# Optimization experiments

Measured on AMD Instinct MI355X. Metric: run time of the kernel, lower is better.

Reference implementation:

```python
import jax, jax.numpy as jnp
import numpy as np

NQ = 4096
N0, N1 = 32768, 8192
N = N0 + N1
F = 128          # emb_dim (32x0e+32x1e)
H = 4            # num_heads
HD = F // H
NB = 64          # fc_neurons[0] radial basis size
DEG = 32
CUTOFFS = jnp.array([2.0, 4.0], dtype=jnp.float32)
OFFSETS = jnp.array([0.1, 0.2], dtype=jnp.float32)


def _sph_harm(u):
    # component-normalized real spherical harmonics l=0,1,2 of unit vectors u [E,3]
    x, y, z = u[:, 0], u[:, 1], u[:, 2]
    s3, s15, s5 = 3.0 ** 0.5, 15.0 ** 0.5, 5.0 ** 0.5
    return jnp.stack([
        jnp.ones_like(x),
        s3 * x, s3 * y, s3 * z,
        s15 * x * y, s15 * y * z, 0.5 * s5 * (3.0 * z * z - 1.0),
        s15 * x * z, 0.5 * s15 * (x * x - y * y),
    ], axis=-1)  # [E,9]


def setup_inputs() -> dict:
    key = jax.random.key(0)
    ks = jax.random.split(key, 20)
    E0 = NQ * DEG
    E1 = NQ * DEG
    edge_src = jnp.concatenate([
        jax.random.randint(ks[0], (E0,), 0, N0),
        jax.random.randint(ks[1], (E1,), N0, N),
    ])
    edge_dst = jnp.concatenate([
        jax.random.randint(ks[2], (E0,), 0, NQ),
        jax.random.randint(ks[3], (E1,), 0, NQ),
    ])
    scale_id = jnp.concatenate([jnp.zeros((E0,), jnp.int32), jnp.ones((E1,), jnp.int32)])
    r = lambda k, sh, s=1.0: jax.random.normal(k, sh, jnp.float32) * s
    return {
        'query_coord': r(ks[4], (NQ, 3)),
        'node_feature': r(ks[5], (N, F)),
        'node_coord': r(ks[6], (N, 3)),
        'edge_src': edge_src, 'edge_dst': edge_dst, 'scale_id': scale_id,
        'b_dst': r(ks[7], (F,)),
        'Wq': r(ks[8], (F, F), F ** -0.5),
        'Wk': r(ks[9], (F, F), F ** -0.5),
        'Wv': r(ks[10], (F, F), F ** -0.5),
        'Wo': r(ks[11], (F, F), F ** -0.5),
        'bo': r(ks[12], (F,)),
        'W_rad0': r(ks[13], (NB, NB), NB ** -0.5), 'b_rad0': r(ks[14], (NB,)),
        'W_rad1': r(ks[15], (NB, NB), NB ** -0.5), 'b_rad1': r(ks[16], (NB,)),
        'W_msg': r(ks[17], (NB, F), NB ** -0.5),
        'W_sh': r(ks[18], (9, F), 9 ** -0.5),
        'W_alpha': r(ks[19], (NB, H), NB ** -0.5),
    }


def _forward(query_coord, node_feature, node_coord, b_dst, Wq, Wk, Wv, Wo, bo,
             W_rad0, b_rad0, W_rad1, b_rad1, W_msg, W_sh, W_alpha,
             edge_src, edge_dst, scale_id):
    Nq = query_coord.shape[0]
    vec = node_coord[edge_src] - query_coord[edge_dst]            # [E,3]
    rlen = jnp.sqrt(jnp.sum(vec * vec, -1) + 1e-12)               # [E]
    off = OFFSETS[scale_id]
    cut = CUTOFFS[scale_id]
    xn = (rlen - off) / (cut - off)                               # normalized radius per scale
    centers = jnp.linspace(0.0, 1.0, NB)
    std = 1.0 / NB
    g = jnp.exp(-0.5 * ((xn[:, None] - centers) / std) ** 2)      # [E,NB] gaussian RBF
    soft = 0.5 * (1.0 + jnp.cos(jnp.pi * jnp.clip((xn - 0.8) / 0.2, 0.0, 1.0)))
    g = g * soft[:, None]                                         # soft finite cutoff
    # per-scale Linear after radial basis (2 scales, masked select)
    edge_scalar = jnp.where((scale_id == 0)[:, None], g @ W_rad0 + b_rad0, g @ W_rad1 + b_rad1)
    sh = _sph_harm(vec / rlen[:, None])                           # [E,9]
    # attention GNN (equiformer-style): dst features start as zeros + learned bias
    q = (b_dst @ Wq).reshape(H, HD)
    k = (node_feature @ Wk)[edge_src].reshape(-1, H, HD)
    logits = jnp.einsum('hd,ehd->eh', q, k) / (HD ** 0.5) + edge_scalar @ W_alpha  # [E,H]
    m = jax.ops.segment_max(logits, edge_dst, num_segments=Nq)
    p = jnp.exp(logits - m[edge_dst])
    denom = jax.ops.segment_sum(p, edge_dst, num_segments=Nq)
    alpha = p / (denom[edge_dst] + 1e-9)                          # segment softmax [E,H]
    v_e = (node_feature @ Wv)[edge_src] * (edge_scalar @ W_msg) + sh @ W_sh  # [E,F]
    msg = (alpha[:, :, None] * v_e.reshape(-1, H, HD)).reshape(-1, F)
    out = jax.ops.segment_sum(msg, edge_dst, num_segments=Nq)     # [Nq,F]
    return out @ Wo + bo


def reference(query_coord, node_feature, node_coord, edge_src, edge_dst, scale_id,
              b_dst, Wq, Wk, Wv, Wo, bo, W_rad0, b_rad0, W_rad1, b_rad1,
              W_msg, W_sh, W_alpha):
    return _forward(query_coord, node_feature, node_coord, b_dst, Wq, Wk, Wv, Wo, bo,
                    W_rad0, b_rad0, W_rad1, b_rad1, W_msg, W_sh, W_alpha,
                    edge_src, edge_dst, scale_id)
```

## Files before the change

### kernel.cpp

```cpp
#include <hip/hip_runtime.h>
#include <hip/hip_bf16.h>
#include <math.h>

#define PI_F 3.14159265358979323846f

typedef __attribute__((ext_vector_type(8))) short short8v;
typedef __attribute__((ext_vector_type(4))) float f32x4;

__device__ __forceinline__ short f2bf(float x) {
    return __builtin_bit_cast(short, __float2bfloat16(x));
}
__device__ __forceinline__ float bf2f(unsigned short u) {
    return __uint_as_float(((unsigned)u) << 16);
}
__device__ __forceinline__ int pack_bf2(float a, float b) {
    return (int)(unsigned short)f2bf(a) | ((int)(unsigned short)f2bf(b) << 16);
}

static const size_t WS_WA     = 0;
static const size_t WS_BA     = 512;
static const size_t WS_BM     = 520;
static const size_t WS_WMF    = 776;
static const size_t WS_WSHF   = 8968;
static const size_t WS_QKF    = 11016;
static const size_t WS_WVF    = 12040;
static const size_t WS_WOF    = 20232;
static const size_t WS_COUNTS = 28424;
static const size_t WS_OFFS   = 36624;
static const size_t WS_CURSOR = 44824;
static const size_t WS_PACKED = 53016;
static const size_t WS_LK     = 315160;
static const size_t WS_EDP    = 479000;
static const size_t WS_EDG    = 1527576;
static const size_t WS_VB     = 2576152;
static const size_t WS_OUTPRE = 5197592;

__global__ __launch_bounds__(256) void k_prepfmt(
    const float* b_dst, const float* Wq, const float* Wk,
    const float* W_rad0, const float* b_rad0,
    const float* W_rad1, const float* b_rad1,
    const float* W_msg, const float* W_alpha, const float* Wv,
    const float* Wo, const float* W_sh,
    const int* edge_dst, const int* scale_id,
    float* Wa, float* ba, float* bm,
    short* WmF, short* WshF, short* QKF, short* WVF, short* WOF,
    int* counts, int E, int NQr) {
    __shared__ float qs_s[128];
    __shared__ float qk_s[512];
    int t = threadIdx.x;
    int b = blockIdx.x;
    if (b == 0) {
        if (t < 128) {
            float acc = 0.f;
            for (int c = 0; c < 128; ++c) acc += b_dst[c] * Wq[c * 128 + t];
            qs_s[t] = acc;
        }
        __syncthreads();
        if (t < 128) {
            const float invs = 0.17677669529663687f;
            for (int h = 0; h < 4; ++h) {
                float acc = 0.f;
                for (int d = 0; d < 32; ++d)
                    acc += Wk[t * 128 + h * 32 + d] * qs_s[h * 32 + d];
                qk_s[t * 4 + h] = acc * invs;
            }
        }
        for (int idx = t; idx < 512; idx += 256) {
            int s = idx >> 8, i = (idx >> 2) & 63, h = idx & 3;
            const float* Wr = s ? W_rad1 : W_rad0;
            float acc = 0.f;
            for (int u = 0; u < 64; ++u) acc += Wr[i * 64 + u] * W_alpha[u * 4 + h];
            Wa[idx] = acc;
        }
        if (t < 8) {
            int s = t >> 2, h = t & 3;
            const float* br = s ? b_rad1 : b_rad0;
            float acc = 0.f;
            for (int u = 0; u < 64; ++u) acc += br[u] * W_alpha[u * 4 + h];
            ba[t] = acc;
        }
        {
            int s = t >> 7, c = t & 127;
            const float* br = s ? b_rad1 : b_rad0;
            float acc = 0.f;
            for (int u = 0; u < 64; ++u) acc += br[u] * W_msg[u * 128 + c];
            bm[t] = acc;
        }
        __syncthreads();
        for (int idx = t; idx < 2048; idx += 256) {
            int j = idx & 7, lane = (idx >> 3) & 63, kh = idx >> 9;
            int k = kh * 32 + ((lane >> 4) << 3) + j;
            int col = lane & 15;
            QKF[idx] = f2bf(col < 4 ? qk_s[k * 4 + col] : 0.f);
        }
    } else if (b <= 208) {
        int item = (b - 1) * 256 + t;
        if (item < 16384) {
            int j = item & 7, lane = (item >> 3) & 63, kh = (item >> 9) & 1;
            int ct = (item >> 10) & 7, sid = item >> 13;
            int k = kh * 32 + ((lane >> 4) << 3) + j;
            int c = (lane & 15) * 8 + ct;
            const float* Wr = sid ? W_rad1 : W_rad0;
            float acc = 0.f;
            for (int u = 0; u < 64; ++u) acc += Wr[k * 64 + u] * W_msg[u * 128 + c];
            WmF[item] = f2bf(acc);
        } else if (item < 20480) {
            int i2 = item - 16384;
            int j = i2 & 7, lane = (i2 >> 3) & 63, ct = (i2 >> 9) & 7;
            int k = ((lane >> 4) << 3) + j;
            int c = (lane & 15) * 8 + ct;
            WshF[i2] = f2bf(k < 9 ? W_sh[k * 128 + c] : 0.f);
        } else if (item < 36864) {
            int i2 = item - 20480;
            int j = i2 & 7, lane = (i2 >> 3) & 63, ct = (i2 >> 9) & 7, kh = (i2 >> 12) & 3;
            int k = kh * 32 + ((lane >> 4) << 3) + j;
            int c = (lane & 15) * 8 + ct;
            WVF[i2] = f2bf(Wv[k * 128 + c]);
        } else {
            int i2 = item - 36864;
            int j = i2 & 7, lane = (i2 >> 3) & 63, ct = (i2 >> 9) & 7, kh = (i2 >> 12) & 3;
            int k = kh * 32 + ((lane >> 4) << 3) + j;
            int c = (lane & 15) * 8 + ct;
            WOF[i2] = f2bf(Wo[k * 128 + c]);
        }
    } else {
        int e = (b - 209) * 256 + t;
        if (e < E) atomicAdd(&counts[scale_id[e] * NQr + edge_dst[e]], 1);
    }
}

template <typename OUT, bool LK>
__global__ __launch_bounds__(256) void k_mgemm(
    const float* A, const short* WF, const float* bias, OUT* out,
    float* lk, const short* QKF, int M) {
    int t = threadIdx.x;
    int w = t >> 6, lane = t & 63;
    int m = lane & 15, grp = lane >> 4;
    int row0 = (blockIdx.x * 4 + w) * 16;
    if (row0 >= M) return;

    short8v a[4];
#pragma unroll
    for (int kh = 0; kh < 4; ++kh) {
        const float* ap = &A[(size_t)(row0 + m) * 128 + kh * 32 + grp * 8];
        float4 f0 = *(const float4*)ap;
        float4 f1 = *(const float4*)(ap + 4);
        a[kh][0] = f2bf(f0.x); a[kh][1] = f2bf(f0.y);
        a[kh][2] = f2bf(f0.z); a[kh][3] = f2bf(f0.w);
        a[kh][4] = f2bf(f1.x); a[kh][5] = f2bf(f1.y);
        a[kh][6] = f2bf(f1.z); a[kh][7] = f2bf(f1.w);
    }
    if constexpr (LK) {
        f32x4 cl = {0.f, 0.f, 0.f, 0.f};
#pragma unroll
        for (int kh = 0; kh < 4; ++kh) {
            short8v qb = *(const short8v*)&QKF[(kh * 64 + lane) * 8];
            cl = __builtin_amdgcn_mfma_f32_16x16x32_bf16(a[kh], qb, cl, 0, 0, 0);
        }
        if (m < 4) {
#pragma unroll
            for (int r = 0; r < 4; ++r)
                lk[(size_t)(row0 + grp * 4 + r) * 4 + m] = cl[r];
        }
    }
    f32x4 c8[8];
#pragma unroll
    for (int ct = 0; ct < 8; ++ct) {
        f32x4 c = {0.f, 0.f, 0.f, 0.f};
#pragma unroll
        for (int kh = 0; kh < 4; ++kh) {
            short8v bf = *(const short8v*)&WF[((kh * 8 + ct) * 64 + lane) * 8];
            c = __builtin_amdgcn_mfma_f32_16x16x32_bf16(a[kh], bf, c, 0, 0, 0);
        }
        c8[ct] = c;
    }
    if constexpr (sizeof(OUT) == 2) {
#pragma unroll
        for (int r = 0; r < 4; ++r) {
            int row = row0 + grp * 4 + r;
            int4 sv;
            sv.x = pack_bf2(c8[0][r], c8[1][r]);
            sv.y = pack_bf2(c8[2][r], c8[3][r]);
            sv.z = pack_bf2(c8[4][r], c8[5][r]);
            sv.w = pack_bf2(c8[6][r], c8[7][r]);
            *(int4*)&out[(size_t)row * 128 + m * 8] = sv;
        }
    } else {
        float4 b0 = make_float4(0.f, 0.f, 0.f, 0.f), b1 = b0;
        if (bias) {
            b0 = *(const float4*)&bias[m * 8];
            b1 = *(const float4*)&bias[m * 8 + 4];
        }
#pragma unroll
        for (int r = 0; r < 4; ++r) {
            int row = row0 + grp * 4 + r;
            float4 o0 = make_float4(c8[0][r] + b0.x, c8[1][r] + b0.y,
                                    c8[2][r] + b0.z, c8[3][r] + b0.w);
            float4 o1 = make_float4(c8[4][r] + b1.x, c8[5][r] + b1.y,
                                    c8[6][r] + b1.z, c8[7][r] + b1.w);
            *(float4*)&out[(size_t)row * 128 + m * 8] = o0;
            *(float4*)&out[(size_t)row * 128 + m * 8 + 4] = o1;
        }
    }
}

__global__ void k_scan(const int* counts, int* offsets, int* cursor, int nkey) {
    __shared__ int sdata[256];
    int t = threadIdx.x;
    int chunk = (nkey + 255) / 256;
    int sum = 0;
    for (int i = 0; i < chunk; ++i) {
        int idx = t * chunk + i;
        sum += (idx < nkey) ? counts[idx] : 0;
    }
    sdata[t] = sum;
    __syncthreads();
    for (int off = 1; off < 256; off <<= 1) {
        int v = (t >= off) ? sdata[t - off] : 0;
        __syncthreads();
        sdata[t] += v;
        __syncthreads();
    }
    int run = sdata[t] - sum;
    for (int i = 0; i < chunk; ++i) {
        int idx = t * chunk + i;
        if (idx < nkey) {
            offsets[idx] = run;
            cursor[idx] = run;
            run += counts[idx];
        }
    }
    if (t == 255) offsets[nkey] = sdata[255];
}

__global__ __launch_bounds__(256) void k_scatter_edge(
    const int* edge_src, const int* edge_dst, const int* scale_id,
    const float* qc, const float* nc, const float* lk,
    const float* WaB, const float* baB, int* cursor,
    int* packed, float* edP, float* edG, int E, int NQr) {
    __shared__ float WaS[512];
    __shared__ float baS[8];
    int t = threadIdx.x;
    for (int i = t; i < 512; i += 256) WaS[i] = WaB[i];
    if (t < 8) baS[t] = baB[t];
    __syncthreads();
    int e = blockIdx.x * 256 + t;
    if (e >= E) return;
    int src = edge_src[e], dst = edge_dst[e], sid = scale_id[e];
    int pos = atomicAdd(&cursor[sid * NQr + dst], 1);

    float qx = qc[dst * 3 + 0], qy = qc[dst * 3 + 1], qz = qc[dst * 3 + 2];
    float vx = nc[src * 3 + 0] - qx;
    float vy = nc[src * 3 + 1] - qy;
    float vz = nc[src * 3 + 2] - qz;
    float r = sqrtf(vx * vx + vy * vy + vz * vz + 1e-12f);
    float rinv = 1.0f / r;
    float ux = vx * rinv, uy = vy * rinv, uz = vz * rinv;

    float roff = sid ? 0.2f : 0.1f;
    float rdiv = sid ? (1.0f / 3.8f) : (1.0f / 1.9f);
    float xn = (r - roff) * rdiv;
    float su = fminf(fmaxf((xn - 0.8f) * 5.0f, 0.0f), 1.0f);
    float soft = 0.5f * (1.0f + __cosf(PI_F * su));

    float4 lkv = *(const float4*)&lk[(size_t)src * 4];

    const float qs = 64.f / 63.f;
    const float Qc = __expf(-qs * qs);
    const float* Wrow = WaS + sid * 256;
    float a0 = 0.f, a1 = 0.f, a2 = 0.f, a3 = 0.f;
#pragma unroll
    for (int ch = 0; ch < 8; ++ch) {
        float d = (xn - (float)(ch * 8) * (1.0f / 63.0f)) * 64.0f;
        float g = __expf(-0.5f * d * d);
        float tt = __expf(fminf(qs * d - 0.5f * qs * qs, 60.f));
#pragma unroll
        for (int j = 0; j < 8; ++j) {
            float4 wa = *(const float4*)&Wrow[(ch * 8 + j) * 4];
            a0 = fmaf(g, wa.x, a0);
            a1 = fmaf(g, wa.y, a1);
            a2 = fmaf(g, wa.z, a2);
            a3 = fmaf(g, wa.w, a3);
            g *= tt; tt *= Qc;
        }
    }
    float p0 = __expf(lkv.x + soft * a0 + baS[sid * 4 + 0]);
    float p1 = __expf(lkv.y + soft * a1 + baS[sid * 4 + 1]);
    float p2 = __expf(lkv.z + soft * a2 + baS[sid * 4 + 2]);
    float p3 = __expf(lkv.w + soft * a3 + baS[sid * 4 + 3]);
    packed[pos] = src | (dst << 16);
    *(float4*)&edP[(size_t)pos * 4] = make_float4(p0, p1, p2, p3);
    *(float4*)&edG[(size_t)pos * 4] = make_float4(ux, uy, uz, xn);
}

__device__ __forceinline__ short8v gchain(float xn, int k0, float soft, float Qc) {
    const float qs = 64.f / 63.f;
    float d = (xn - (float)k0 * (1.0f / 63.0f)) * 64.0f;
    float g = __expf(-0.5f * d * d);
    float tt = __expf(fminf(qs * d - 0.5f * qs * qs, 60.f));
    short8v rr;
#pragma unroll
    for (int j = 0; j < 8; ++j) {
        rr[j] = f2bf(g * soft);
        g *= tt; tt *= Qc;
    }
    return rr;
}

__global__ __launch_bounds__(256) void k_main7(
    const int* offsets, const int* packed, const float* edP, const float* edG,
    const unsigned short* Vu, const float* bm, const short* WmF, const short* WshF,
    float* out_pre, int NQr) {
    int t = threadIdx.x;
    int w = t >> 6, lane = t & 63;
    int dst = blockIdx.x * 4 + w;
    if (dst >= NQr) return;
    int m = lane & 15, grp = lane >> 4;
    int h = m >> 2;

    int s0a = offsets[dst],       s1a = offsets[dst + 1];
    int s0b = offsets[NQr + dst], s1b = offsets[NQr + dst + 1];
    int nt0 = (s1a - s0a + 15) >> 4;
    int nt1 = (s1b - s0b + 15) >> 4;
    int ntot = nt0 + nt1;

    float acc[8];
#pragma unroll
    for (int i = 0; i < 8; ++i) acc[i] = 0.f;
    float den = 0.f;

    float4 bmA0 = *(const float4*)&bm[m * 8];
    float4 bmA1 = *(const float4*)&bm[m * 8 + 4];
    float4 bmB0 = *(const float4*)&bm[128 + m * 8];
    float4 bmB1 = *(const float4*)&bm[128 + m * 8 + 4];

    const float qs = 64.f / 63.f;
    const float Qc = __expf(-qs * qs);
    const float s3 = 1.7320508075688772f, s15 = 3.872983346207417f, s5 = 2.23606797749979f;

    if (ntot > 0) {
        auto load_tile = [&](int tl, int& sid_o, float4& G4o, float (&pho)[4], int4 (&vvo)[4]) {
            int sid = (tl >= nt0) ? 1 : 0;
            int q0  = sid ? (s0b + (tl - nt0) * 16) : (s0a + tl * 16);
            int lim = sid ? s1b : s1a;
            int posA = q0 + m; if (posA >= lim) posA = lim - 1;
            G4o = *(const float4*)&edG[(size_t)posA * 4];
            int srcs[4];
#pragma unroll
            for (int r = 0; r < 4; ++r) {
                int pos = q0 + grp * 4 + r;
                bool valid = pos < lim;
                if (!valid) pos = lim - 1;
                srcs[r] = packed[pos] & 0xFFFF;
                float p = edP[(size_t)pos * 4 + h];
                pho[r] = valid ? p : 0.f;
            }
#pragma unroll
            for (int r = 0; r < 4; ++r)
                vvo[r] = *(const int4*)&Vu[(size_t)srcs[r] * 128 + m * 8];
            sid_o = sid;
        };

        int sidc; float4 G4c; float phc[4]; int4 vvc[4];
        load_tile(0, sidc, G4c, phc, vvc);

        for (int tl = 0; tl < ntot; ++tl) {
            bool hasNext = (tl + 1) < ntot;
            int sidn; float4 G4n; float phn[4]; int4 vvn[4];
            if (hasNext) load_tile(tl + 1, sidn, G4n, phn, vvn);

            int wds[4][4] = {{vvc[0].x, vvc[0].y, vvc[0].z, vvc[0].w},
                             {vvc[1].x, vvc[1].y, vvc[1].z, vvc[1].w},
                             {vvc[2].x, vvc[2].y, vvc[2].z, vvc[2].w},
                             {vvc[3].x, vvc[3].y, vvc[3].z, vvc[3].w}};
            den += phc[0] + phc[1] + phc[2] + phc[3];

            float bmv[8];
            {
                float4 b0 = sidc ? bmB0 : bmA0;
                float4 b1 = sidc ? bmB1 : bmA1;
                bmv[0] = b0.x; bmv[1] = b0.y; bmv[2] = b0.z; bmv[3] = b0.w;
                bmv[4] = b1.x; bmv[5] = b1.y; bmv[6] = b1.z; bmv[7] = b1.w;
            }
            const short* wmp = WmF + sidc * 8192;

            float xn = G4c.w;
            float su = fminf(fmaxf((xn - 0.8f) * 5.0f, 0.0f), 1.0f);
            float soft = 0.5f * (1.0f + __cosf(PI_F * su));
            short8v aG0 = gchain(xn, grp * 8, soft, Qc);
            short8v aG1 = gchain(xn, 32 + grp * 8, soft, Qc);

            float ux = G4c.x, uy = G4c.y, uz = G4c.z;
            float sh[9];
            sh[0] = 1.f; sh[1] = s3 * ux; sh[2] = s3 * uy; sh[3] = s3 * uz;
            sh[4] = s15 * ux * uy; sh[5] = s15 * uy * uz;
            sh[6] = 0.5f * s5 * (3.f * uz * uz - 1.f);
            sh[7] = s15 * ux * uz; sh[8] = 0.5f * s15 * (ux * ux - uy * uy);
            short8v aS;
#pragma unroll
            for (int j = 0; j < 8; ++j) {
                float v = (grp == 0) ? sh[j] : ((grp == 1 && j == 0) ? sh[8] : 0.f);
                aS[j] = f2bf(v);
            }

#pragma unroll
            for (int ct = 0; ct < 8; ++ct) {
                short8v b0 = *(const short8v*)&wmp[((ct * 2 + 0) * 64 + lane) * 8];
                short8v b1 = *(const short8v*)&wmp[((ct * 2 + 1) * 64 + lane) * 8];
                short8v bS = *(const short8v*)&WshF[(ct * 64 + lane) * 8];
                f32x4 cms = {0.f, 0.f, 0.f, 0.f};
                cms = __builtin_amdgcn_mfma_f32_16x16x32_bf16(aG0, b0, cms, 0, 0, 0);
                cms = __builtin_amdgcn_mfma_f32_16x16x32_bf16(aG1, b1, cms, 0, 0, 0);
                f32x4 csh = {0.f, 0.f, 0.f, 0.f};
                csh = __builtin_amdgcn_mfma_f32_16x16x32_bf16(aS, bS, csh, 0, 0, 0);
#pragma unroll
                for (int r = 0; r < 4; ++r) {
                    int word = wds[r][ct >> 1];
                    unsigned short vu = (ct & 1) ? (unsigned short)(word >> 16)
                                                 : (unsigned short)(word & 0xFFFF);
                    float vf = bf2f(vu);
                    float ve = fmaf(vf, cms[r] + bmv[ct], csh[r]);
                    acc[ct] = fmaf(phc[r], ve, acc[ct]);
                }
            }

            if (hasNext) {
                sidc = sidn; G4c = G4n;
#pragma unroll
                for (int r = 0; r < 4; ++r) { phc[r] = phn[r]; vvc[r] = vvn[r]; }
            }
        }
    }

#pragma unroll
    for (int i = 0; i < 8; ++i) {
        acc[i] += __shfl_xor(acc[i], 16);
        acc[i] += __shfl_xor(acc[i], 32);
    }
    den += __shfl_xor(den, 16);
    den += __shfl_xor(den, 32);
    if (lane < 16) {
        float dinv = 1.0f / (den + 1e-9f);
        float4 o0 = make_float4(acc[0] * dinv, acc[1] * dinv, acc[2] * dinv, acc[3] * dinv);
        float4 o1 = make_float4(acc[4] * dinv, acc[5] * dinv, acc[6] * dinv, acc[7] * dinv);
        *(float4*)&out_pre[(size_t)dst * 128 + m * 8] = o0;
        *(float4*)&out_pre[(size_t)dst * 128 + m * 8 + 4] = o1;
    }
}

extern "C" void kernel_launch(void* const* d_in, const int* in_sizes, int n_in,
                              void* d_out, int out_size, void* d_ws, size_t ws_size,
                              hipStream_t stream) {
    const float* query_coord = (const float*)d_in[0];
    const float* node_feature = (const float*)d_in[1];
    const float* node_coord = (const float*)d_in[2];
    const int* edge_src = (const int*)d_in[3];
    const int* edge_dst = (const int*)d_in[4];
    const int* scale_id = (const int*)d_in[5];
    const float* b_dst = (const float*)d_in[6];
    const float* Wq = (const float*)d_in[7];
    const float* Wk = (const float*)d_in[8];
    const float* Wv = (const float*)d_in[9];
    const float* Wo = (const float*)d_in[10];
    const float* bo = (const float*)d_in[11];
    const float* W_rad0 = (const float*)d_in[12];
    const float* b_rad0 = (const float*)d_in[13];
    const float* W_rad1 = (const float*)d_in[14];
    const float* b_rad1 = (const float*)d_in[15];
    const float* W_msg = (const float*)d_in[16];
    const float* W_sh = (const float*)d_in[17];
    const float* W_alpha = (const float*)d_in[18];
    (void)n_in; (void)ws_size; (void)out_size;

    int NQr = in_sizes[0] / 3;
    int Nn = in_sizes[1] / 128;
    int E = in_sizes[3];
    int nkey = NQr * 2;

    float* ws = (float*)d_ws;
    float* Wa = ws + WS_WA;
    float* ba = ws + WS_BA;
    float* bm = ws + WS_BM;
    short* WmF = (short*)(ws + WS_WMF);
    short* WshF = (short*)(ws + WS_WSHF);
    short* QKF = (short*)(ws + WS_QKF);
    short* WVF = (short*)(ws + WS_WVF);
    short* WOF = (short*)(ws + WS_WOF);
    int* counts = (int*)(ws + WS_COUNTS);
    int* offsets = (int*)(ws + WS_OFFS);
    int* cursor = (int*)(ws + WS_CURSOR);
    int* packed = (int*)(ws + WS_PACKED);
    float* lk = ws + WS_LK;
    float* edP = ws + WS_EDP;
    float* edG = ws + WS_EDG;
    unsigned short* Vb = (unsigned short*)(ws + WS_VB);
    float* out_pre = ws + WS_OUTPRE;
    float* out = (float*)d_out;

    hipMemsetAsync(counts, 0, nkey * sizeof(int), stream);
    int histBlocks = (E + 255) / 256;
    hipLaunchKernelGGL(k_prepfmt, dim3(209 + histBlocks), dim3(256), 0, stream,
                       b_dst, Wq, Wk, W_rad0, b_rad0, W_rad1, b_rad1, W_msg, W_alpha,
                       Wv, Wo, W_sh, edge_dst, scale_id,
                       Wa, ba, bm, WmF, WshF, QKF, WVF, WOF, counts, E, NQr);
    hipLaunchKernelGGL((k_mgemm<unsigned short, true>), dim3((Nn + 63) / 64), dim3(256), 0,
                       stream, node_feature, WVF, (const float*)nullptr, Vb, lk, QKF, Nn);
    hipLaunchKernelGGL(k_scan, dim3(1), dim3(256), 0, stream, counts, offsets, cursor, nkey);
    hipLaunchKernelGGL(k_scatter_edge, dim3((E + 255) / 256), dim3(256), 0, stream,
                       edge_src, edge_dst, scale_id, query_coord, node_coord, lk,
                       Wa, ba, cursor, packed, edP, edG, E, NQr);
    hipLaunchKernelGGL(k_main7, dim3((NQr + 3) / 4), dim3(256), 0, stream,
                       offsets, packed, edP, edG, Vb, bm, WmF, WshF, out_pre, NQr);
    hipLaunchKernelGGL((k_mgemm<float, false>), dim3((NQr + 63) / 64), dim3(256), 0, stream,
                       out_pre, WOF, bo, out, (float*)nullptr, (const short*)nullptr, NQr);
}
```

Before: 147.0 us.

## Split per-destination edge loop into independent 16-edge tiles with atomic accumulation

```diff
diff --git a/kernel.cpp b/kernel.cpp
--- a/kernel.cpp
+++ b/kernel.cpp
@@ -28,12 +28,15 @@
 static const size_t WS_COUNTS = 28424;
 static const size_t WS_OFFS   = 36624;
 static const size_t WS_CURSOR = 44824;
-static const size_t WS_PACKED = 53016;
-static const size_t WS_LK     = 315160;
-static const size_t WS_EDP    = 479000;
-static const size_t WS_EDG    = 1527576;
-static const size_t WS_VB     = 2576152;
-static const size_t WS_OUTPRE = 5197592;
+static const size_t WS_TCNT   = 53016;
+static const size_t WS_TMAP   = 53024;
+static const size_t WS_PACKED = 77608;
+static const size_t WS_LK     = 339752;
+static const size_t WS_EDP    = 503592;
+static const size_t WS_EDG    = 1552168;
+static const size_t WS_VB     = 2600744;
+static const size_t WS_OACC   = 5222184;
+static const size_t WS_DACC   = 5746472;
 
 __global__ __launch_bounds__(256) void k_prepfmt(
     const float* b_dst, const float* Wq, const float* Wk,
@@ -129,26 +132,36 @@
     }
 }
 
-template <typename OUT, bool LK>
+template <typename OUT, bool LK, bool DIV>
 __global__ __launch_bounds__(256) void k_mgemm(
     const float* A, const short* WF, const float* bias, OUT* out,
-    float* lk, const short* QKF, int M) {
+    float* lk, const short* QKF, const float* den, int M) {
     int t = threadIdx.x;
     int w = t >> 6, lane = t & 63;
     int m = lane & 15, grp = lane >> 4;
     int row0 = (blockIdx.x * 4 + w) * 16;
     if (row0 >= M) return;
 
+    float dinv[4] = {1.f, 1.f, 1.f, 1.f};
+    if constexpr (DIV) {
+        float4 dv = *(const float4*)&den[(size_t)(row0 + m) * 4];
+        dinv[0] = 1.f / (dv.x + 1e-9f);
+        dinv[1] = 1.f / (dv.y + 1e-9f);
+        dinv[2] = 1.f / (dv.z + 1e-9f);
+        dinv[3] = 1.f / (dv.w + 1e-9f);
+    }
+
     short8v a[4];
 #pragma unroll
     for (int kh = 0; kh < 4; ++kh) {
         const float* ap = &A[(size_t)(row0 + m) * 128 + kh * 32 + grp * 8];
         float4 f0 = *(const float4*)ap;
         float4 f1 = *(const float4*)(ap + 4);
-        a[kh][0] = f2bf(f0.x); a[kh][1] = f2bf(f0.y);
-        a[kh][2] = f2bf(f0.z); a[kh][3] = f2bf(f0.w);
-        a[kh][4] = f2bf(f1.x); a[kh][5] = f2bf(f1.y);
-        a[kh][6] = f2bf(f1.z); a[kh][7] = f2bf(f1.w);
+        float s = dinv[kh];
+        a[kh][0] = f2bf(f0.x * s); a[kh][1] = f2bf(f0.y * s);
+        a[kh][2] = f2bf(f0.z * s); a[kh][3] = f2bf(f0.w * s);
+        a[kh][4] = f2bf(f1.x * s); a[kh][5] = f2bf(f1.y * s);
+        a[kh][6] = f2bf(f1.z * s); a[kh][7] = f2bf(f1.w * s);
     }
     if constexpr (LK) {
         f32x4 cl = {0.f, 0.f, 0.f, 0.f};
@@ -204,16 +217,19 @@
     }
 }
 
-__global__ void k_scan(const int* counts, int* offsets, int* cursor, int nkey) {
+__global__ void k_scan(const int* counts, int* offsets, int* cursor,
+                       int* tcnt, int* tileMap, int nkey) {
     __shared__ int sdata[256];
     int t = threadIdx.x;
     int chunk = (nkey + 255) / 256;
-    int sum = 0;
+    int se = 0, st = 0;
     for (int i = 0; i < chunk; ++i) {
         int idx = t * chunk + i;
-        sum += (idx < nkey) ? counts[idx] : 0;
-    }
-    sdata[t] = sum;
+        int c = (idx < nkey) ? counts[idx] : 0;
+        se += c;
+        st += (c + 15) >> 4;
+    }
+    sdata[t] = se;
     __syncthreads();
     for (int off = 1; off < 256; off <<= 1) {
         int v = (t >= off) ? sdata[t - off] : 0;
@@ -221,16 +237,32 @@
         sdata[t] += v;
         __syncthreads();
     }
-    int run = sdata[t] - sum;
+    int run_e = sdata[t] - se;
+    int tot_e = sdata[255];
+    __syncthreads();
+    sdata[t] = st;
+    __syncthreads();
+    for (int off = 1; off < 256; off <<= 1) {
+        int v = (t >= off) ? sdata[t - off] : 0;
+        __syncthreads();
+        sdata[t] += v;
+        __syncthreads();
+    }
+    int run_t = sdata[t] - st;
+    int tot_t = sdata[255];
     for (int i = 0; i < chunk; ++i) {
         int idx = t * chunk + i;
         if (idx < nkey) {
-            offsets[idx] = run;
-            cursor[idx] = run;
-            run += counts[idx];
-        }
-    }
-    if (t == 255) offsets[nkey] = sdata[255];
+            int c = counts[idx];
+            offsets[idx] = run_e;
+            cursor[idx] = run_e;
+            int nt = (c + 15) >> 4;
+            for (int j = 0; j < nt; ++j) tileMap[run_t + j] = idx | (j << 16);
+            run_e += c;
+            run_t += nt;
+        }
+    }
+    if (t == 0) { offsets[nkey] = tot_e; tcnt[0] = tot_t; }
 }
 
 __global__ __launch_bounds__(256) void k_scatter_edge(
@@ -307,128 +339,93 @@
     return rr;
 }
 
-__global__ __launch_bounds__(256) void k_main7(
+__global__ __launch_bounds__(256) void k_main8(
     const int* offsets, const int* packed, const float* edP, const float* edG,
     const unsigned short* Vu, const float* bm, const short* WmF, const short* WshF,
-    float* out_pre, int NQr) {
+    const int* tcnt, const int* tileMap,
+    float* out_acc, float* den_acc, int NQr) {
     int t = threadIdx.x;
     int w = t >> 6, lane = t & 63;
-    int dst = blockIdx.x * 4 + w;
-    if (dst >= NQr) return;
+    int T = blockIdx.x * 4 + w;
+    if (T >= tcnt[0]) return;
+    int mt = tileMap[T];
+    int key = mt & 0xFFFF, ti = mt >> 16;
+    int sid = (key >= NQr) ? 1 : 0;
+    int dst = key - (sid ? NQr : 0);
+    int q0 = offsets[key] + ti * 16;
+    int lim = offsets[key + 1];
     int m = lane & 15, grp = lane >> 4;
     int h = m >> 2;
 
-    int s0a = offsets[dst],       s1a = offsets[dst + 1];
-    int s0b = offsets[NQr + dst], s1b = offsets[NQr + dst + 1];
-    int nt0 = (s1a - s0a + 15) >> 4;
-    int nt1 = (s1b - s0b + 15) >> 4;
-    int ntot = nt0 + nt1;
-
-    float acc[8];
-#pragma unroll
-    for (int i = 0; i < 8; ++i) acc[i] = 0.f;
-    float den = 0.f;
-
-    float4 bmA0 = *(const float4*)&bm[m * 8];
-    float4 bmA1 = *(const float4*)&bm[m * 8 + 4];
-    float4 bmB0 = *(const float4*)&bm[128 + m * 8];
-    float4 bmB1 = *(const float4*)&bm[128 + m * 8 + 4];
+    int posA = q0 + m; if (posA >= lim) posA = lim - 1;
+    float4 G4 = *(const float4*)&edG[(size_t)posA * 4];
+    int srcs[4]; float ph[4];
+#pragma unroll
+    for (int r = 0; r < 4; ++r) {
+        int pos = q0 + grp * 4 + r;
+        bool valid = pos < lim;
+        if (!valid) pos = lim - 1;
+        srcs[r] = packed[pos] & 0xFFFF;
+        float p = edP[(size_t)pos * 4 + h];
+        ph[r] = valid ? p : 0.f;
+    }
+    int wds[4][4];
+#pragma unroll
+    for (int r = 0; r < 4; ++r) {
+        int4 vv = *(const int4*)&Vu[(size_t)srcs[r] * 128 + m * 8];
+        wds[r][0] = vv.x; wds[r][1] = vv.y; wds[r][2] = vv.z; wds[r][3] = vv.w;
+    }
+
+    float4 bm0 = *(const float4*)&bm[sid * 128 + m * 8];
+    float4 bm1 = *(const float4*)&bm[sid * 128 + m * 8 + 4];
+    float bmv[8] = {bm0.x, bm0.y, bm0.z, bm0.w, bm1.x, bm1.y, bm1.z, bm1.w};
+    const short* wmp = WmF + sid * 8192;
 
     const float qs = 64.f / 63.f;
     const float Qc = __expf(-qs * qs);
+    float xn = G4.w;
+    float su = fminf(fmaxf((xn - 0.8f) * 5.0f, 0.0f), 1.0f);
+    float soft = 0.5f * (1.0f + __cosf(PI_F * su));
+    short8v aG0 = gchain(xn, grp * 8, soft, Qc);
+    short8v aG1 = gchain(xn, 32 + grp * 8, soft, Qc);
+
     const float s3 = 1.7320508075688772f, s15 = 3.872983346207417f, s5 = 2.23606797749979f;
-
-    if (ntot > 0) {
-        auto load_tile = [&](int tl, int& sid_o, float4& G4o, float (&pho)[4], int4 (&vvo)[4]) {
-            int sid = (tl >= nt0) ? 1 : 0;
-            int q0  = sid ? (s0b + (tl - nt0) * 16) : (s0a + tl * 16);
-            int lim = sid ? s1b : s1a;
-            int posA = q0 + m; if (posA >= lim) posA = lim - 1;
-            G4o = *(const float4*)&edG[(size_t)posA * 4];
-            int srcs[4];
-#pragma unroll
-            for (int r = 0; r < 4; ++r) {
-                int pos = q0 + grp * 4 + r;
-                bool valid = pos < lim;
-                if (!valid) pos = lim - 1;
-                srcs[r] = packed[pos] & 0xFFFF;
-                float p = edP[(size_t)pos * 4 + h];
-                pho[r] = valid ? p : 0.f;
-            }
-#pragma unroll
-            for (int r = 0; r < 4; ++r)
-                vvo[r] = *(const int4*)&Vu[(size_t)srcs[r] * 128 + m * 8];
-            sid_o = sid;
-        };
-
-        int sidc; float4 G4c; float phc[4]; int4 vvc[4];
-        load_tile(0, sidc, G4c, phc, vvc);
-
-        for (int tl = 0; tl < ntot; ++tl) {
-            bool hasNext = (tl + 1) < ntot;
-            int sidn; float4 G4n; float phn[4]; int4 vvn[4];
-            if (hasNext) load_tile(tl + 1, sidn, G4n, phn, vvn);
-
-            int wds[4][4] = {{vvc[0].x, vvc[0].y, vvc[0].z, vvc[0].w},
-                             {vvc[1].x, vvc[1].y, vvc[1].z, vvc[1].w},
-                             {vvc[2].x, vvc[2].y, vvc[2].z, vvc[2].w},
-                             {vvc[3].x, vvc[3].y, vvc[3].z, vvc[3].w}};
-            den += phc[0] + phc[1] + phc[2] + phc[3];
-
-            float bmv[8];
-            {
-                float4 b0 = sidc ? bmB0 : bmA0;
-                float4 b1 = sidc ? bmB1 : bmA1;
-                bmv[0] = b0.x; bmv[1] = b0.y; bmv[2] = b0.z; bmv[3] = b0.w;
-                bmv[4] = b1.x; bmv[5] = b1.y; bmv[6] = b1.z; bmv[7] = b1.w;
-            }
-            const short* wmp = WmF + sidc * 8192;
-
-            float xn = G4c.w;
-            float su = fminf(fmaxf((xn - 0.8f) * 5.0f, 0.0f), 1.0f);
-            float soft = 0.5f * (1.0f + __cosf(PI_F * su));
-            short8v aG0 = gchain(xn, grp * 8, soft, Qc);
-            short8v aG1 = gchain(xn, 32 + grp * 8, soft, Qc);
-
-            float ux = G4c.x, uy = G4c.y, uz = G4c.z;
-            float sh[9];
-            sh[0] = 1.f; sh[1] = s3 * ux; sh[2] = s3 * uy; sh[3] = s3 * uz;
-            sh[4] = s15 * ux * uy; sh[5] = s15 * uy * uz;
-            sh[6] = 0.5f * s5 * (3.f * uz * uz - 1.f);
-            sh[7] = s15 * ux * uz; sh[8] = 0.5f * s15 * (ux * ux - uy * uy);
-            short8v aS;
-#pragma unroll
-            for (int j = 0; j < 8; ++j) {
-                float v = (grp == 0) ? sh[j] : ((grp == 1 && j == 0) ? sh[8] : 0.f);
-                aS[j] = f2bf(v);
-            }
-
-#pragma unroll
-            for (int ct = 0; ct < 8; ++ct) {
-                short8v b0 = *(const short8v*)&wmp[((ct * 2 + 0) * 64 + lane) * 8];
-                short8v b1 = *(const short8v*)&wmp[((ct * 2 + 1) * 64 + lane) * 8];
-                short8v bS = *(const short8v*)&WshF[(ct * 64 + lane) * 8];
-                f32x4 cms = {0.f, 0.f, 0.f, 0.f};
-                cms = __builtin_amdgcn_mfma_f32_16x16x32_bf16(aG0, b0, cms, 0, 0, 0);
-                cms = __builtin_amdgcn_mfma_f32_16x16x32_bf16(aG1, b1, cms, 0, 0, 0);
-                f32x4 csh = {0.f, 0.f, 0.f, 0.f};
-                csh = __builtin_amdgcn_mfma_f32_16x16x32_bf16(aS, bS, csh, 0, 0, 0);
-#pragma unroll
-                for (int r = 0; r < 4; ++r) {
-                    int word = wds[r][ct >> 1];
-                    unsigned short vu = (ct & 1) ? (unsigned short)(word >> 16)
-                                                 : (unsigned short)(word & 0xFFFF);
-                    float vf = bf2f(vu);
-                    float ve = fmaf(vf, cms[r] + bmv[ct], csh[r]);
-                    acc[ct] = fmaf(phc[r], ve, acc[ct]);
-                }
-            }
-
-            if (hasNext) {
-                sidc = sidn; G4c = G4n;
-#pragma unroll
-                for (int r = 0; r < 4; ++r) { phc[r] = phn[r]; vvc[r] = vvn[r]; }
-            }
+    float ux = G4.x, uy = G4.y, uz = G4.z;
+    float sh[9];
+    sh[0] = 1.f; sh[1] = s3 * ux; sh[2] = s3 * uy; sh[3] = s3 * uz;
+    sh[4] = s15 * ux * uy; sh[5] = s15 * uy * uz;
+    sh[6] = 0.5f * s5 * (3.f * uz * uz - 1.f);
+    sh[7] = s15 * ux * uz; sh[8] = 0.5f * s15 * (ux * ux - uy * uy);
+    short8v aS;
+#pragma unroll
+    for (int j = 0; j < 8; ++j) {
+        float v = (grp == 0) ? sh[j] : ((grp == 1 && j == 0) ? sh[8] : 0.f);
+        aS[j] = f2bf(v);
+    }
+
+    float acc[8];
+#pragma unroll
+    for (int i = 0; i < 8; ++i) acc[i] = 0.f;
+    float den = ph[0] + ph[1] + ph[2] + ph[3];
+
+#pragma unroll
+    for (int ct = 0; ct < 8; ++ct) {
+        short8v b0 = *(const short8v*)&wmp[((ct * 2 + 0) * 64 + lane) * 8];
+        short8v b1 = *(const short8v*)&wmp[((ct * 2 + 1) * 64 + lane) * 8];
+        short8v bS = *(const short8v*)&WshF[(ct * 64 + lane) * 8];
+        f32x4 cms = {bmv[ct], bmv[ct], bmv[ct], bmv[ct]};
+        cms = __builtin_amdgcn_mfma_f32_16x16x32_bf16(aG0, b0, cms, 0, 0, 0);
+        cms = __builtin_amdgcn_mfma_f32_16x16x32_bf16(aG1, b1, cms, 0, 0, 0);
+        f32x4 csh = {0.f, 0.f, 0.f, 0.f};
+        csh = __builtin_amdgcn_mfma_f32_16x16x32_bf16(aS, bS, csh, 0, 0, 0);
+#pragma unroll
+        for (int r = 0; r < 4; ++r) {
+            int wd = wds[r][ct >> 1];
+            unsigned short vu = (ct & 1) ? (unsigned short)(wd >> 16)
+                                         : (unsigned short)(wd & 0xFFFF);
+            float vf = bf2f(vu);
+            float ve = fmaf(vf, cms[r], csh[r]);
+            acc[ct] = fmaf(ph[r], ve, acc[ct]);
         }
     }
 
@@ -440,11 +437,11 @@
     den += __shfl_xor(den, 16);
     den += __shfl_xor(den, 32);
     if (lane < 16) {
-        float dinv = 1.0f / (den + 1e-9f);
-        float4 o0 = make_float4(acc[0] * dinv, acc[1] * dinv, acc[2] * dinv, acc[3] * dinv);
-        float4 o1 = make_float4(acc[4] * dinv, acc[5] * dinv, acc[6] * dinv, acc[7] * dinv);
-        *(float4*)&out_pre[(size_t)dst * 128 + m * 8] = o0;
-        *(float4*)&out_pre[(size_t)dst * 128 + m * 8 + 4] = o1;
+#pragma unroll
+        for (int ct = 0; ct < 8; ++ct)
+            unsafeAtomicAdd(&out_acc[(size_t)dst * 128 + m * 8 + ct], acc[ct]);
+        if ((m & 3) == 0)
+            unsafeAtomicAdd(&den_acc[(size_t)dst * 4 + h], den);
     }
 }
 
@@ -489,28 +486,38 @@
     int* counts = (int*)(ws + WS_COUNTS);
     int* offsets = (int*)(ws + WS_OFFS);
     int* cursor = (int*)(ws + WS_CURSOR);
+    int* tcnt = (int*)(ws + WS_TCNT);
+    int* tileMap = (int*)(ws + WS_TMAP);
     int* packed = (int*)(ws + WS_PACKED);
     float* lk = ws + WS_LK;
     float* edP = ws + WS_EDP;
     float* edG = ws + WS_EDG;
     unsigned short* Vb = (unsigned short*)(ws + WS_VB);
-    float* out_pre = ws + WS_OUTPRE;
+    float* out_acc = ws + WS_OACC;
+    float* den_acc = ws + WS_DACC;
     float* out = (float*)d_out;
 
     hipMemsetAsync(counts, 0, nkey * sizeof(int), stream);
+    hipMemsetAsync(out_acc, 0, (size_t)(NQr * 128 + NQr * 4) * sizeof(float), stream);
     int histBlocks = (E + 255) / 256;
     hipLaunchKernelGGL(k_prepfmt, dim3(209 + histBlocks), dim3(256), 0, stream,
                        b_dst, Wq, Wk, W_rad0, b_rad0, W_rad1, b_rad1, W_msg, W_alpha,
                        Wv, Wo, W_sh, edge_dst, scale_id,
                        Wa, ba, bm, WmF, WshF, QKF, WVF, WOF, counts, E, NQr);
-    hipLaunchKernelGGL((k_mgemm<unsigned short, true>), dim3((Nn + 63) / 64), dim3(256), 0,
-                       stream, node_feature, WVF, (const float*)nullptr, Vb, lk, QKF, Nn);
-    hipLaunchKernelGGL(k_scan, dim3(1), dim3(256), 0, stream, counts, offsets, cursor, nkey);
+    hipLaunchKernelGGL((k_mgemm<unsigned short, true, false>), dim3((Nn + 63) / 64),
+                       dim3(256), 0, stream,
+                       node_feature, WVF, (const float*)nullptr, Vb, lk, QKF,
+                       (const float*)nullptr, Nn);
+    hipLaunchKernelGGL(k_scan, dim3(1), dim3(256), 0, stream,
+                       counts, offsets, cursor, tcnt, tileMap, nkey);
     hipLaunchKernelGGL(k_scatter_edge, dim3((E + 255) / 256), dim3(256), 0, stream,
                        edge_src, edge_dst, scale_id, query_coord, node_coord, lk,
                        Wa, ba, cursor, packed, edP, edG, E, NQr);
-    hipLaunchKernelGGL(k_main7, dim3((NQr + 3) / 4), dim3(256), 0, stream,
-                       offsets, packed, edP, edG, Vb, bm, WmF, WshF, out_pre, NQr);
-    hipLaunchKernelGGL((k_mgemm<float, false>), dim3((NQr + 63) / 64), dim3(256), 0, stream,
-                       out_pre, WOF, bo, out, (float*)nullptr, (const short*)nullptr, NQr);
-}
+    int maxTiles = E / 16 + nkey;
+    hipLaunchKernelGGL(k_main8, dim3((maxTiles + 3) / 4), dim3(256), 0, stream,
+                       offsets, packed, edP, edG, Vb, bm, WmF, WshF,
+                       tcnt, tileMap, out_acc, den_acc, NQr);
+    hipLaunchKernelGGL((k_mgemm<float, false, true>), dim3((NQr + 63) / 64), dim3(256), 0,
+                       stream, out_acc, WOF, bo, out, (float*)nullptr,
+                       (const short*)nullptr, den_acc, NQr);
+}
```

Result: slower. 197.4 us (+34.3%).

## Split each query across two waves by scale and deepen gather prefetch

Applied to the files above, without the earlier changes.

```diff
diff --git a/kernel.cpp b/kernel.cpp
--- a/kernel.cpp
+++ b/kernel.cpp
@@ -307,90 +307,85 @@
     return rr;
 }
 
-__global__ __launch_bounds__(256) void k_main7(
+__global__ __launch_bounds__(256) void k_main10(
     const int* offsets, const int* packed, const float* edP, const float* edG,
     const unsigned short* Vu, const float* bm, const short* WmF, const short* WshF,
     float* out_pre, int NQr) {
+    __shared__ float part[4][132];
     int t = threadIdx.x;
     int w = t >> 6, lane = t & 63;
-    int dst = blockIdx.x * 4 + w;
-    if (dst >= NQr) return;
+    int sid = w & 1;
+    int dst = blockIdx.x * 2 + (w >> 1);
     int m = lane & 15, grp = lane >> 4;
     int h = m >> 2;
 
-    int s0a = offsets[dst],       s1a = offsets[dst + 1];
-    int s0b = offsets[NQr + dst], s1b = offsets[NQr + dst + 1];
-    int nt0 = (s1a - s0a + 15) >> 4;
-    int nt1 = (s1b - s0b + 15) >> 4;
-    int ntot = nt0 + nt1;
+    int key = sid * NQr + dst;
+    int s0 = offsets[key], s1 = offsets[key + 1];
+    int nt = (s1 - s0 + 15) >> 4;
 
     float acc[8];
 #pragma unroll
     for (int i = 0; i < 8; ++i) acc[i] = 0.f;
     float den = 0.f;
 
-    float4 bmA0 = *(const float4*)&bm[m * 8];
-    float4 bmA1 = *(const float4*)&bm[m * 8 + 4];
-    float4 bmB0 = *(const float4*)&bm[128 + m * 8];
-    float4 bmB1 = *(const float4*)&bm[128 + m * 8 + 4];
+    float4 bm0 = *(const float4*)&bm[sid * 128 + m * 8];
+    float4 bm1 = *(const float4*)&bm[sid * 128 + m * 8 + 4];
+    float bmv[8] = {bm0.x, bm0.y, bm0.z, bm0.w, bm1.x, bm1.y, bm1.z, bm1.w};
+    const short* wmp = WmF + sid * 8192;
 
     const float qs = 64.f / 63.f;
     const float Qc = __expf(-qs * qs);
     const float s3 = 1.7320508075688772f, s15 = 3.872983346207417f, s5 = 2.23606797749979f;
 
-    if (ntot > 0) {
-        auto load_tile = [&](int tl, int& sid_o, float4& G4o, float (&pho)[4], int4 (&vvo)[4]) {
-            int sid = (tl >= nt0) ? 1 : 0;
-            int q0  = sid ? (s0b + (tl - nt0) * 16) : (s0a + tl * 16);
-            int lim = sid ? s1b : s1a;
-            int posA = q0 + m; if (posA >= lim) posA = lim - 1;
-            G4o = *(const float4*)&edG[(size_t)posA * 4];
-            int srcs[4];
+    if (nt > 0) {
+        auto loadA = [&](int tl, int (&srcs)[4], float (&ph)[4], float4& G4) {
+            int q0 = s0 + tl * 16;
+            int posA = q0 + m; if (posA >= s1) posA = s1 - 1;
+            G4 = *(const float4*)&edG[(size_t)posA * 4];
 #pragma unroll
             for (int r = 0; r < 4; ++r) {
                 int pos = q0 + grp * 4 + r;
-                bool valid = pos < lim;
-                if (!valid) pos = lim - 1;
+                bool valid = pos < s1;
+                if (!valid) pos = s1 - 1;
                 srcs[r] = packed[pos] & 0xFFFF;
                 float p = edP[(size_t)pos * 4 + h];
-                pho[r] = valid ? p : 0.f;
+                ph[r] = valid ? p : 0.f;
             }
+        };
+        auto loadV = [&](const int (&srcs)[4], int4 (&vv)[4]) {
 #pragma unroll
             for (int r = 0; r < 4; ++r)
-                vvo[r] = *(const int4*)&Vu[(size_t)srcs[r] * 128 + m * 8];
-            sid_o = sid;
+                vv[r] = *(const int4*)&Vu[(size_t)srcs[r] * 128 + m * 8];
         };
 
-        int sidc; float4 G4c; float phc[4]; int4 vvc[4];
-        load_tile(0, sidc, G4c, phc, vvc);
-
-        for (int tl = 0; tl < ntot; ++tl) {
-            bool hasNext = (tl + 1) < ntot;
-            int sidn; float4 G4n; float phn[4]; int4 vvn[4];
-            if (hasNext) load_tile(tl + 1, sidn, G4n, phn, vvn);
-
-            int wds[4][4] = {{vvc[0].x, vvc[0].y, vvc[0].z, vvc[0].w},
-                             {vvc[1].x, vvc[1].y, vvc[1].z, vvc[1].w},
-                             {vvc[2].x, vvc[2].y, vvc[2].z, vvc[2].w},
-                             {vvc[3].x, vvc[3].y, vvc[3].z, vvc[3].w}};
-            den += phc[0] + phc[1] + phc[2] + phc[3];
-
-            float bmv[8];
-            {
-                float4 b0 = sidc ? bmB0 : bmA0;
-                float4 b1 = sidc ? bmB1 : bmA1;
-                bmv[0] = b0.x; bmv[1] = b0.y; bmv[2] = b0.z; bmv[3] = b0.w;
-                bmv[4] = b1.x; bmv[5] = b1.y; bmv[6] = b1.z; bmv[7] = b1.w;
+        int srcsA[4], srcsB[4], srcsC[4];
+        float phA[4], phB[4], phC[4];
+        float4 gA, gB, gC;
+        int4 vA[4], vB[4];
+
+        loadA(0, srcsA, phA, gA);
+        loadV(srcsA, vA);
+        if (nt > 1) loadA(1, srcsB, phB, gB);
+
+        for (int tl = 0; tl < nt; ++tl) {
+            if (tl + 1 < nt) loadV(srcsB, vB);
+            if (tl + 2 < nt) loadA(tl + 2, srcsC, phC, gC);
+
+            int wds[4][4];
+#pragma unroll
+            for (int r = 0; r < 4; ++r) {
+                wds[r][0] = vA[r].x; wds[r][1] = vA[r].y;
+                wds[r][2] = vA[r].z; wds[r][3] = vA[r].w;
             }
-            const short* wmp = WmF + sidc * 8192;
-
-            float xn = G4c.w;
+            den += phA[0] + phA[1] + phA[2] + phA[3];
+
+            float xn = gA.w;
             float su = fminf(fmaxf((xn - 0.8f) * 5.0f, 0.0f), 1.0f);
             float soft = 0.5f * (1.0f + __cosf(PI_F * su));
             short8v aG0 = gchain(xn, grp * 8, soft, Qc);
             short8v aG1 = gchain(xn, 32 + grp * 8, soft, Qc);
 
-            float ux = G4c.x, uy = G4c.y, uz = G4c.z;
+            float ux = gA.x, uy = gA.y, uz = gA.z;
             float sh[9];
             sh[0] = 1.f; sh[1] = s3 * ux; sh[2] = s3 * uy; sh[3] = s3 * uz;
             sh[4] = s15 * ux * uy; sh[5] = s15 * uy * uz;
@@ -408,26 +403,28 @@
                 short8v b0 = *(const short8v*)&wmp[((ct * 2 + 0) * 64 + lane) * 8];
                 short8v b1 = *(const short8v*)&wmp[((ct * 2 + 1) * 64 + lane) * 8];
                 short8v bS = *(const short8v*)&WshF[(ct * 64 + lane) * 8];
-                f32x4 cms = {0.f, 0.f, 0.f, 0.f};
+                f32x4 cms = {bmv[ct], bmv[ct], bmv[ct], bmv[ct]};
                 cms = __builtin_amdgcn_mfma_f32_16x16x32_bf16(aG0, b0, cms, 0, 0, 0);
                 cms = __builtin_amdgcn_mfma_f32_16x16x32_bf16(aG1, b1, cms, 0, 0, 0);
                 f32x4 csh = {0.f, 0.f, 0.f, 0.f};
                 csh = __builtin_amdgcn_mfma_f32_16x16x32_bf16(aS, bS, csh, 0, 0, 0);
 #pragma unroll
                 for (int r = 0; r < 4; ++r) {
-                    int word = wds[r][ct >> 1];
-                    unsigned short vu = (ct & 1) ? (unsigned short)(word >> 16)
-                                                 : (unsigned short)(word & 0xFFFF);
+                    int wd = wds[r][ct >> 1];
+                    unsigned short vu = (ct & 1) ? (unsigned short)(wd >> 16)
+                                                 : (unsigned short)(wd & 0xFFFF);
                     float vf = bf2f(vu);
-                    float ve = fmaf(vf, cms[r] + bmv[ct], csh[r]);
-                    acc[ct] = fmaf(phc[r], ve, acc[ct]);
+                    float ve = fmaf(vf, cms[r], csh[r]);
+                    acc[ct] = fmaf(phA[r], ve, acc[ct]);
                 }
             }
 
-            if (hasNext) {
-                sidc = sidn; G4c = G4n;
-#pragma unroll
-                for (int r = 0; r < 4; ++r) { phc[r] = phn[r]; vvc[r] = vvn[r]; }
+            gA = gB; gB = gC;
+#pragma unroll
+            for (int r = 0; r < 4; ++r) {
+                phA[r] = phB[r]; phB[r] = phC[r];
+                srcsB[r] = srcsC[r];
+                vA[r] = vB[r];
             }
         }
     }
@@ -440,11 +437,22 @@
     den += __shfl_xor(den, 16);
     den += __shfl_xor(den, 32);
     if (lane < 16) {
-        float dinv = 1.0f / (den + 1e-9f);
-        float4 o0 = make_float4(acc[0] * dinv, acc[1] * dinv, acc[2] * dinv, acc[3] * dinv);
-        float4 o1 = make_float4(acc[4] * dinv, acc[5] * dinv, acc[6] * dinv, acc[7] * dinv);
-        *(float4*)&out_pre[(size_t)dst * 128 + m * 8] = o0;
-        *(float4*)&out_pre[(size_t)dst * 128 + m * 8 + 4] = o1;
+#pragma unroll
+        for (int ct = 0; ct < 8; ++ct) part[w][m * 8 + ct] = acc[ct];
+        if ((m & 3) == 0) part[w][128 + h] = den;
+    }
+    __syncthreads();
+
+    {
+        int which = t >> 7;
+        int col = t & 127;
+        int d2 = blockIdx.x * 2 + which;
+        if (d2 < NQr) {
+            int hh = col >> 5;
+            float s = part[2 * which][col] + part[2 * which + 1][col];
+            float d = part[2 * which][128 + hh] + part[2 * which + 1][128 + hh];
+            out_pre[(size_t)d2 * 128 + col] = s / (d + 1e-9f);
+        }
     }
 }
 
@@ -509,7 +517,7 @@
     hipLaunchKernelGGL(k_scatter_edge, dim3((E + 255) / 256), dim3(256), 0, stream,
                        edge_src, edge_dst, scale_id, query_coord, node_coord, lk,
                        Wa, ba, cursor, packed, edP, edG, E, NQr);
-    hipLaunchKernelGGL(k_main7, dim3((NQr + 3) / 4), dim3(256), 0, stream,
+    hipLaunchKernelGGL(k_main10, dim3((NQr + 1) / 2), dim3(256), 0, stream,
                        offsets, packed, edP, edG, Vb, bm, WmF, WshF, out_pre, NQr);
     hipLaunchKernelGGL((k_mgemm<float, false>), dim3((NQr + 63) / 64), dim3(256), 0, stream,
                        out_pre, WOF, bo, out, (float*)nullptr, (const short*)nullptr, NQr);
```

Result: faster. 129.7 us (-11.7%).
